# Optimization experiments

Measured on AMD Instinct MI355X. Metric: run time of the kernel, lower is better.

Reference implementation:

```python
import jax, jax.numpy as jnp
import numpy as np

ALPHA = 0.1          # dt / tau = 10 / 100
HIDDEN_NOISE = 0.1   # std of per-step hidden noise


def setup_inputs() -> dict:
    key = jax.random.key(0)
    k1, k2, k3, k4, k5 = jax.random.split(key, 5)
    B, T, I, H, O = 128, 800, 9, 1024, 8
    x = jax.random.normal(k1, (B, T, I), dtype=jnp.float32)
    noise = jax.random.normal(k2, (B, T, H), dtype=jnp.float32)
    # xavier/kaiming-like scaled Gaussian init for the weight matrices
    Win = jax.random.normal(k3, (H, I), dtype=jnp.float32) * (1.0 / np.sqrt(I))
    Wrec = jax.random.normal(k4, (H, H), dtype=jnp.float32) * (1.0 / np.sqrt(H))
    Wout = jax.random.normal(k5, (O, H), dtype=jnp.float32) * (1.0 / np.sqrt(H))
    return {"x": x, "noise": noise, "Win": Win, "Wrec": Wrec, "Wout": Wout}


def reference(x, noise, Win, Wrec, Wout):
    # Precompute input drive for all timesteps: it + noise  -> [B, T, H]
    drive = jnp.einsum('bti,hi->bth', x, Win) + HIDDEN_NOISE * noise
    B = x.shape[0]
    H = Wrec.shape[0]
    h0 = jnp.zeros((B, H), dtype=x.dtype)

    def step(h, d):  # d: [B, H] drive at time t
        pre = d + h @ Wrec.T
        h_new = jax.nn.relu(pre) * ALPHA + (1.0 - ALPHA) * h
        return h_new, h_new

    _, hs = jax.lax.scan(step, h0, jnp.swapaxes(drive, 0, 1))  # hs: [T, B, H]
    hiddens = jnp.swapaxes(hs, 0, 1)                            # [B, T, H]
    logits = jnp.einsum('bth,oh->bto', hiddens, Wout)           # [B, T, O]
    outs = jax.nn.softmax(logits, axis=-1)
    return hiddens, outs
```

## Files before the change

kernel.cpp:

```cpp
#include <hip/hip_runtime.h>

#define B_TOT 128
#define T_LEN 800
#define I_DIM 9
#define H_DIM 1024
#define O_DIM 8
#define NB    16
#define NSLC  8
#define NCOL  128
#define GROUPS (B_TOT / NB)

typedef float f32x4 __attribute__((ext_vector_type(4)));
typedef short s16x8 __attribute__((ext_vector_type(8)));
typedef unsigned long long u64;

#define TAGM 0x0000800000008000ull

__device__ __forceinline__ unsigned short f2bf(float f) {
    unsigned u = __float_as_uint(f);
    u += 0x7fffu + ((u >> 16) & 1u);
    return (unsigned short)(u >> 16);
}

#define AL(p) __hip_atomic_load((p), __ATOMIC_RELAXED, __HIP_MEMORY_SCOPE_AGENT)
#define AS(p, v) __hip_atomic_store((p), (v), __ATOMIC_RELAXED, __HIP_MEMORY_SCOPE_AGENT)

__device__ __forceinline__ int swz(int s, int r) {
    return s ^ ((s >> 3) & 7) ^ (r & 7);
}

__global__ __launch_bounds__(512, 1)
void rnn_scan(const float* __restrict__ x,
              const float* __restrict__ noise,
              const float* __restrict__ Win,
              const float* __restrict__ Wrec,
              unsigned short* __restrict__ hx,
              float* __restrict__ hiddens)
{
    __shared__ __align__(16) char hlds[2][NB * 2048];
    __shared__ float xs[2][NB][I_DIM];
    __shared__ int strd[2][NSLC];

    const int tid  = threadIdx.x;
    const int lane = tid & 63;
    const int w    = tid >> 6;
    const int g    = blockIdx.x & 7;
    const int s    = blockIdx.x >> 3;
    const int b0   = g * NB;
    const int l15  = lane & 15;
    const int kb   = lane >> 4;
    const int n    = s * NCOL + w * 16 + l15;

    s16x8 breg[32];
    {
        const float* wrow = Wrec + (size_t)n * H_DIM + kb * 8;
#pragma unroll
        for (int kt = 0; kt < 32; ++kt) {
            float4 v0 = *(const float4*)(wrow + kt * 32);
            float4 v1 = *(const float4*)(wrow + kt * 32 + 4);
            union { s16x8 v; unsigned short u[8]; } r;
            r.u[0] = f2bf(v0.x); r.u[1] = f2bf(v0.y); r.u[2] = f2bf(v0.z); r.u[3] = f2bf(v0.w);
            r.u[4] = f2bf(v1.x); r.u[5] = f2bf(v1.y); r.u[6] = f2bf(v1.z); r.u[7] = f2bf(v1.w);
            breg[kt] = r.v;
        }
    }

    float win[I_DIM];
#pragma unroll
    for (int i = 0; i < I_DIM; ++i) win[i] = Win[n * I_DIM + i];

    unsigned short* hxg = hx + (size_t)g * (2 * NB * H_DIM);

    const int grow = lane >> 2;
    const int gq   = lane & 3;

    if (tid < 2 * NSLC) ((int*)strd)[tid] = 0;
    float hreg[4] = {0.f, 0.f, 0.f, 0.f};
    __syncthreads();

#pragma unroll 1
    for (int t = 0; t < T_LEN; ++t) {
        const int pb = t & 1;

        if (tid < NB * I_DIM) {
            int b = tid / I_DIM, i = tid - b * I_DIM;
            xs[pb][b][i] = x[((size_t)(b0 + b) * T_LEN + t) * I_DIM + i];
        }
        float nz[4];
#pragma unroll
        for (int r = 0; r < 4; ++r)
            nz[r] = noise[((size_t)(b0 + kb * 4 + r) * T_LEN + t) * H_DIM + n];

        f32x4 acc0 = {0.f, 0.f, 0.f, 0.f}, acc1 = {0.f, 0.f, 0.f, 0.f};

        if (t == 0) {
            __syncthreads();
        } else {
            const u64 exp = (((t - 1) >> 1) & 1) ? TAGM : 0ull;
            const u64* sp = (const u64*)(hxg + ((t - 1) & 1) * (NB * H_DIM))
                            + grow * 256 + w * 32 + gq * 2;
            u64 v[8];
#pragma unroll
            for (int j = 0; j < 4; ++j) {
                v[2 * j]     = AL(sp + j * 8);
                v[2 * j + 1] = AL(sp + j * 8 + 1);
            }
            for (;;) {
                u64 bad = 0;
#pragma unroll
                for (int j = 0; j < 8; ++j) bad |= (v[j] ^ exp) & TAGM;
                if (__all(bad == 0)) break;
#pragma unroll
                for (int j = 0; j < 4; ++j) {
                    if ((((v[2 * j] ^ exp) | (v[2 * j + 1] ^ exp)) & TAGM) != 0) {
                        v[2 * j]     = AL(sp + j * 8);
                        v[2 * j + 1] = AL(sp + j * 8 + 1);
                    }
                }
            }
            char* drow = hlds[pb] + grow * 2048;
#pragma unroll
            for (int j = 0; j < 4; ++j) {
                ulonglong2 q2;
                q2.x = v[2 * j] & ~TAGM;
                q2.y = v[2 * j + 1] & ~TAGM;
                *(ulonglong2*)(drow + swz(w * 16 + gq + j * 4, grow) * 16) = q2;
            }
            if (lane == 0)
                __hip_atomic_store(&strd[pb][w], t, __ATOMIC_RELEASE,
                                   __HIP_MEMORY_SCOPE_WORKGROUP);

            const char* rrow = hlds[pb] + l15 * 2048;
#pragma unroll
            for (int j = 0; j < 8; ++j) {
                if (j != w) {
                    while (__hip_atomic_load(&strd[pb][j], __ATOMIC_ACQUIRE,
                                             __HIP_MEMORY_SCOPE_WORKGROUP) < t) {}
                }
#pragma unroll
                for (int kk = 0; kk < 4; kk += 2) {
                    const int kt = 4 * j + kk;
                    s16x8 a0 = *(const s16x8*)(rrow + swz(4 * kt + kb, l15) * 16);
                    acc0 = __builtin_amdgcn_mfma_f32_16x16x32_bf16(a0, breg[kt], acc0, 0, 0, 0);
                    s16x8 a1 = *(const s16x8*)(rrow + swz(4 * kt + 4 + kb, l15) * 16);
                    acc1 = __builtin_amdgcn_mfma_f32_16x16x32_bf16(a1, breg[kt + 1], acc1, 0, 0, 0);
                }
            }
        }
        const f32x4 acc = acc0 + acc1;

        float xd[4];
#pragma unroll
        for (int r = 0; r < 4; ++r) {
            float sx = 0.f;
#pragma unroll
            for (int i = 0; i < I_DIM; ++i) sx += win[i] * xs[pb][kb * 4 + r][i];
            xd[r] = sx;
        }

#pragma unroll
        for (int r = 0; r < 4; ++r) {
            const float pre = acc[r] + xd[r] + 0.1f * nz[r];
            hreg[r] = 0.9f * hreg[r] + 0.1f * fmaxf(pre, 0.f);
        }

        const unsigned tagbit = (unsigned)((t >> 1) & 1) << 15;
        unsigned* hdst32 = (unsigned*)(hxg + pb * (NB * H_DIM));
#pragma unroll
        for (int r = 0; r < 4; ++r) {
            unsigned self  = f2bf(hreg[r]);
            unsigned other = __shfl_xor(self, 1, 64);
            if (!(l15 & 1))
                AS(hdst32 + (kb * 4 + r) * (H_DIM / 2) + (n >> 1),
                   self | (other << 16) | tagbit);
        }
        asm volatile("" ::: "memory");

#pragma unroll
        for (int r = 0; r < 4; ++r)
            __builtin_nontemporal_store(
                hreg[r], &hiddens[((size_t)(b0 + kb * 4 + r) * T_LEN + t) * H_DIM + n]);

        __syncthreads();
    }
}

__global__ __launch_bounds__(256)
void out_head(const float* __restrict__ hiddens, const float* __restrict__ Wout,
              float* __restrict__ outs)
{
    __shared__ float wlds[O_DIM][H_DIM];
    const int tid = threadIdx.x;
    for (int j = tid; j < (O_DIM * H_DIM) / 4; j += 256)
        ((float4*)wlds)[j] = ((const float4*)Wout)[j];
    __syncthreads();

    const int wave = tid >> 6, lane = tid & 63;
#pragma unroll
    for (int rr = 0; rr < 2; ++rr) {
        const size_t row = (size_t)blockIdx.x * 8 + wave * 2 + rr;
        const float* hp = hiddens + row * H_DIM;

        float a0=0,a1=0,a2=0,a3=0,a4=0,a5=0,a6=0,a7=0;
#pragma unroll
        for (int j = 0; j < 4; ++j) {
            float4 hv = *(const float4*)(hp + lane * 4 + j * 256);
#define DOT(o, acc) { float4 wv = *(const float4*)&wlds[o][lane*4 + j*256]; \
                      acc += hv.x*wv.x + hv.y*wv.y + hv.z*wv.z + hv.w*wv.w; }
            DOT(0,a0) DOT(1,a1) DOT(2,a2) DOT(3,a3)
            DOT(4,a4) DOT(5,a5) DOT(6,a6) DOT(7,a7)
#undef DOT
        }
#pragma unroll
        for (int off = 32; off; off >>= 1) {
            a0 += __shfl_xor(a0, off, 64); a1 += __shfl_xor(a1, off, 64);
            a2 += __shfl_xor(a2, off, 64); a3 += __shfl_xor(a3, off, 64);
            a4 += __shfl_xor(a4, off, 64); a5 += __shfl_xor(a5, off, 64);
            a6 += __shfl_xor(a6, off, 64); a7 += __shfl_xor(a7, off, 64);
        }
        if (lane == 0) {
            float mx = fmaxf(fmaxf(fmaxf(a0,a1),fmaxf(a2,a3)),
                             fmaxf(fmaxf(a4,a5),fmaxf(a6,a7)));
            float e0=expf(a0-mx), e1=expf(a1-mx), e2=expf(a2-mx), e3=expf(a3-mx);
            float e4=expf(a4-mx), e5=expf(a5-mx), e6=expf(a6-mx), e7=expf(a7-mx);
            float inv = 1.f / (e0+e1+e2+e3+e4+e5+e6+e7);
            float* op = outs + row * O_DIM;
            op[0]=e0*inv; op[1]=e1*inv; op[2]=e2*inv; op[3]=e3*inv;
            op[4]=e4*inv; op[5]=e5*inv; op[6]=e6*inv; op[7]=e7*inv;
        }
    }
}

extern "C" void kernel_launch(void* const* d_in, const int* in_sizes, int n_in,
                              void* d_out, int out_size, void* d_ws, size_t ws_size,
                              hipStream_t stream) {
    const float* x     = (const float*)d_in[0];
    const float* noise = (const float*)d_in[1];
    const float* Win   = (const float*)d_in[2];
    const float* Wrec  = (const float*)d_in[3];
    const float* Wout  = (const float*)d_in[4];

    float* hiddens = (float*)d_out;
    float* outs    = hiddens + (size_t)B_TOT * T_LEN * H_DIM;

    unsigned short* hx = (unsigned short*)d_ws;

    rnn_scan<<<GROUPS * NSLC, 512, 0, stream>>>(x, noise, Win, Wrec, hx, hiddens);
    out_head<<<(B_TOT * T_LEN) / 8, 256, 0, stream>>>(hiddens, Wout, outs);
}
```

Before: 3.475 ms.

## Precompute input drive in separate kernel and drop per-step block barrier

Adds a pre_drive kernel that computes Win·x + 0.1·noise for every timestep and writes it into the hiddens output buffer. The recurrent scan then reads this drive in place, overwrites it with h, and no longer does per-step x staging in shared memory or the input projection. It also removes the end-of-step __syncthreads and relies on the per-wave LDS flags, indexing the LDS buffer by (t-1)&1. This takes the input projection and one block barrier off the serial critical path, at the cost of an extra full write and read of a B*T*H buffer and a possible LDS reuse race without the barrier.

```diff
diff --git a/kernel.cpp b/kernel.cpp
--- a/kernel.cpp
+++ b/kernel.cpp
@@ -29,17 +29,46 @@
     return s ^ ((s >> 3) & 7) ^ (r & 7);
 }
 
+__global__ __launch_bounds__(256)
+void pre_drive(const float* __restrict__ x, const float* __restrict__ noise,
+               const float* __restrict__ Win, float* __restrict__ drive)
+{
+    const int tid = threadIdx.x;
+    const int h4  = tid * 4;
+    float w[4][I_DIM];
+#pragma unroll
+    for (int q = 0; q < 4; ++q)
+#pragma unroll
+        for (int i = 0; i < I_DIM; ++i) w[q][i] = Win[(h4 + q) * I_DIM + i];
+
+#pragma unroll 1
+    for (int bt = blockIdx.x; bt < B_TOT * T_LEN; bt += gridDim.x) {
+        float xv[I_DIM];
+#pragma unroll
+        for (int i = 0; i < I_DIM; ++i) xv[i] = x[bt * I_DIM + i];
+        float4 nz = *(const float4*)(noise + (size_t)bt * H_DIM + h4);
+        float d[4];
+#pragma unroll
+        for (int q = 0; q < 4; ++q) {
+            float s = 0.f;
+#pragma unroll
+            for (int i = 0; i < I_DIM; ++i) s += w[q][i] * xv[i];
+            d[q] = s;
+        }
+        float4 dv;
+        dv.x = d[0] + 0.1f * nz.x;  dv.y = d[1] + 0.1f * nz.y;
+        dv.z = d[2] + 0.1f * nz.z;  dv.w = d[3] + 0.1f * nz.w;
+        *(float4*)(drive + (size_t)bt * H_DIM + h4) = dv;
+    }
+}
+
 __global__ __launch_bounds__(512, 1)
-void rnn_scan(const float* __restrict__ x,
-              const float* __restrict__ noise,
-              const float* __restrict__ Win,
-              const float* __restrict__ Wrec,
+void rnn_scan(const float* __restrict__ Wrec,
               unsigned short* __restrict__ hx,
               float* __restrict__ hiddens)
 {
     __shared__ __align__(16) char hlds[2][NB * 2048];
-    __shared__ float xs[2][NB][I_DIM];
-    __shared__ int strd[2][NSLC];
+    __shared__ int strd[NSLC];
 
     const int tid  = threadIdx.x;
     const int lane = tid & 63;
@@ -65,37 +94,25 @@
         }
     }
 
-    float win[I_DIM];
-#pragma unroll
-    for (int i = 0; i < I_DIM; ++i) win[i] = Win[n * I_DIM + i];
-
     unsigned short* hxg = hx + (size_t)g * (2 * NB * H_DIM);
 
     const int grow = lane >> 2;
     const int gq   = lane & 3;
 
-    if (tid < 2 * NSLC) ((int*)strd)[tid] = 0;
+    if (tid < NSLC) strd[tid] = 0;
     float hreg[4] = {0.f, 0.f, 0.f, 0.f};
     __syncthreads();
 
 #pragma unroll 1
     for (int t = 0; t < T_LEN; ++t) {
-        const int pb = t & 1;
-
-        if (tid < NB * I_DIM) {
-            int b = tid / I_DIM, i = tid - b * I_DIM;
-            xs[pb][b][i] = x[((size_t)(b0 + b) * T_LEN + t) * I_DIM + i];
-        }
-        float nz[4];
+        float drv[4];
 #pragma unroll
         for (int r = 0; r < 4; ++r)
-            nz[r] = noise[((size_t)(b0 + kb * 4 + r) * T_LEN + t) * H_DIM + n];
+            drv[r] = hiddens[((size_t)(b0 + kb * 4 + r) * T_LEN + t) * H_DIM + n];
 
         f32x4 acc0 = {0.f, 0.f, 0.f, 0.f}, acc1 = {0.f, 0.f, 0.f, 0.f};
 
-        if (t == 0) {
-            __syncthreads();
-        } else {
+        if (t > 0) {
             const u64 exp = (((t - 1) >> 1) & 1) ? TAGM : 0ull;
             const u64* sp = (const u64*)(hxg + ((t - 1) & 1) * (NB * H_DIM))
                             + grow * 256 + w * 32 + gq * 2;
@@ -118,7 +135,7 @@
                     }
                 }
             }
-            char* drow = hlds[pb] + grow * 2048;
+            char* drow = hlds[(t - 1) & 1] + grow * 2048;
 #pragma unroll
             for (int j = 0; j < 4; ++j) {
                 ulonglong2 q2;
@@ -127,14 +144,14 @@
                 *(ulonglong2*)(drow + swz(w * 16 + gq + j * 4, grow) * 16) = q2;
             }
             if (lane == 0)
-                __hip_atomic_store(&strd[pb][w], t, __ATOMIC_RELEASE,
+                __hip_atomic_store(&strd[w], t, __ATOMIC_RELEASE,
                                    __HIP_MEMORY_SCOPE_WORKGROUP);
 
-            const char* rrow = hlds[pb] + l15 * 2048;
+            const char* rrow = hlds[(t - 1) & 1] + l15 * 2048;
 #pragma unroll
             for (int j = 0; j < 8; ++j) {
                 if (j != w) {
-                    while (__hip_atomic_load(&strd[pb][j], __ATOMIC_ACQUIRE,
+                    while (__hip_atomic_load(&strd[j], __ATOMIC_ACQUIRE,
                                              __HIP_MEMORY_SCOPE_WORKGROUP) < t) {}
                 }
 #pragma unroll
@@ -149,23 +166,14 @@
         }
         const f32x4 acc = acc0 + acc1;
 
-        float xd[4];
 #pragma unroll
         for (int r = 0; r < 4; ++r) {
-            float sx = 0.f;
-#pragma unroll
-            for (int i = 0; i < I_DIM; ++i) sx += win[i] * xs[pb][kb * 4 + r][i];
-            xd[r] = sx;
-        }
-
-#pragma unroll
-        for (int r = 0; r < 4; ++r) {
-            const float pre = acc[r] + xd[r] + 0.1f * nz[r];
+            const float pre = acc[r] + drv[r];
             hreg[r] = 0.9f * hreg[r] + 0.1f * fmaxf(pre, 0.f);
         }
 
         const unsigned tagbit = (unsigned)((t >> 1) & 1) << 15;
-        unsigned* hdst32 = (unsigned*)(hxg + pb * (NB * H_DIM));
+        unsigned* hdst32 = (unsigned*)(hxg + (t & 1) * (NB * H_DIM));
 #pragma unroll
         for (int r = 0; r < 4; ++r) {
             unsigned self  = f2bf(hreg[r]);
@@ -180,8 +188,6 @@
         for (int r = 0; r < 4; ++r)
             __builtin_nontemporal_store(
                 hreg[r], &hiddens[((size_t)(b0 + kb * 4 + r) * T_LEN + t) * H_DIM + n]);
-
-        __syncthreads();
     }
 }
 
@@ -245,6 +251,7 @@
 
     unsigned short* hx = (unsigned short*)d_ws;
 
-    rnn_scan<<<GROUPS * NSLC, 512, 0, stream>>>(x, noise, Win, Wrec, hx, hiddens);
+    pre_drive<<<2048, 256, 0, stream>>>(x, noise, Win, hiddens);
+    rnn_scan<<<GROUPS * NSLC, 512, 0, stream>>>(Wrec, hx, hiddens);
     out_head<<<(B_TOT * T_LEN) / 8, 256, 0, stream>>>(hiddens, Wout, outs);
 }
```

Measured after the change: 4.217 ms. 21.3% more time.
